# Kernel tuning notes

Hardware: AMD Instinct MI355X
Metric: run time of the kernel (lower is better)

The kernel has to match this reference:

```python
import jax, jax.numpy as jnp
import numpy as np
from jax import lax

BETA = 0.9
THRESHOLD = 1.0
SLOPE = 25.0
TIME_STEPS = 50


@jax.custom_vjp
def spike(u):
    # Heaviside forward; fast_sigmoid surrogate backward
    return (u > 0).astype(u.dtype)

def _spike_fwd(u):
    return spike(u), u

def _spike_bwd(u, g):
    return (g / (SLOPE * jnp.abs(u) + 1.0) ** 2,)

spike.defvjp(_spike_fwd, _spike_bwd)


def setup_inputs() -> dict:
    key = jax.random.key(0)
    k = jax.random.split(key, 5)
    B, D_IN, D_H, D_OUT = 1024, 1024, 2048, 256
    return {
        "x": jax.random.normal(k[0], (B, D_IN), jnp.float32),
        "W1": jax.random.normal(k[1], (D_H, D_IN), jnp.float32) / np.sqrt(D_IN),
        "b1": jax.random.normal(k[2], (D_H,), jnp.float32) * 0.01,
        "W2": jax.random.normal(k[3], (D_OUT, D_H), jnp.float32) / np.sqrt(D_H),
        "b2": jax.random.normal(k[4], (D_OUT,), jnp.float32) * 0.01,
    }


def reference(x, W1, b1, W2, b2):
    # fc1(x) is constant across time steps (static input) -> hoist out of scan
    cur1 = x @ W1.T + b1  # [B, H]
    B = x.shape[0]
    H, O = W1.shape[0], W2.shape[0]
    dt = x.dtype

    def step(carry, _):
        mem1, mem2, h_sum, out_sum = carry
        # snntorch Leaky, subtract reset: reset based on PREVIOUS mem, detached
        reset1 = lax.stop_gradient((mem1 > THRESHOLD).astype(dt))
        mem1 = BETA * mem1 + cur1 - reset1 * THRESHOLD
        spk1 = spike(mem1 - THRESHOLD)
        cur2 = spk1 @ W2.T + b2  # [B, O]
        reset2 = lax.stop_gradient((mem2 > THRESHOLD).astype(dt))
        mem2 = BETA * mem2 + cur2 - reset2 * THRESHOLD
        spk2 = spike(mem2 - THRESHOLD)
        return (mem1, mem2, h_sum + spk1, out_sum + spk2), None

    init = (jnp.zeros((B, H), dt), jnp.zeros((B, O), dt),
            jnp.zeros((B, H), dt), jnp.zeros((B, O), dt))
    (mem1, mem2, h_sum, out_sum), _ = lax.scan(step, init, None, length=TIME_STEPS)
    return (h_sum, out_sum)
```

## Files before the change

kernel.cpp:

```cpp
#include <hip/hip_runtime.h>
#include <stdint.h>


#define BATCH 1024
#define DIN   1024
#define DH    2048
#define DOUT  256
#define TSTEPS 50
#define QS    131072.0f
#define QINVS 7.62939453125e-6f

typedef __bf16 bf16x8 __attribute__((ext_vector_type(8)));
typedef float  f32x4  __attribute__((ext_vector_type(4)));
typedef int    i32x4  __attribute__((ext_vector_type(4)));
typedef int    i32x16 __attribute__((ext_vector_type(16)));

__device__ __forceinline__ uint16_t f32_bf16_rne(float f) {
  uint32_t u = __float_as_uint(f);
  uint32_t r = u + 0x7FFFu + ((u >> 16) & 1u);
  return (uint16_t)(r >> 16);
}

__device__ __forceinline__ i32x4 expand16(uint32_t s) {
  i32x4 r;
  r[0] = (int)((( s        & 0xFu) * 0x00204081u) & 0x01010101u);
  r[1] = (int)((((s >>  4) & 0xFu) * 0x00204081u) & 0x01010101u);
  r[2] = (int)((((s >>  8) & 0xFu) * 0x00204081u) & 0x01010101u);
  r[3] = (int)((((s >> 12) & 0xFu) * 0x00204081u) & 0x01010101u);
  return r;
}

__global__ void prep_kernel(const float* __restrict__ x, const float* __restrict__ W1,
                            const float* __restrict__ W2,
                            uint16_t* __restrict__ PXh, uint16_t* __restrict__ PXl,
                            uint16_t* __restrict__ PWh, uint16_t* __restrict__ PWl,
                            int8_t* __restrict__ PB) {
  int bid = blockIdx.x;
  if (bid < 1536) {
    const float* src;
    uint16_t *dh, *dl;
    int m, ko; size_t M;
    if (bid < 512) {
      int t = bid * 256 + threadIdx.x;
      m = t & 1023; ko = t >> 10; M = 1024;
      src = x + (size_t)m * DIN + ko * 8;
      dh = PXh; dl = PXl;
    } else {
      int t = (bid - 512) * 256 + threadIdx.x;
      m = t & 2047; ko = t >> 11; M = 2048;
      src = W1 + (size_t)m * DIN + ko * 8;
      dh = PWh; dl = PWl;
    }
    float4 a = *(const float4*)(src);
    float4 b = *(const float4*)(src + 4);
    float v[8] = {a.x, a.y, a.z, a.w, b.x, b.y, b.z, b.w};
    uint16_t h[8], l[8];
#pragma unroll
    for (int j = 0; j < 8; ++j) {
      h[j] = f32_bf16_rne(v[j]);
      l[j] = f32_bf16_rne(v[j] - __uint_as_float((uint32_t)h[j] << 16));
    }
    size_t o = ((size_t)ko * M + m) * 8;
    *(uint4*)(dh + o) = make_uint4(h[0] | (h[1] << 16), h[2] | (h[3] << 16),
                                   h[4] | (h[5] << 16), h[6] | (h[7] << 16));
    *(uint4*)(dl + o) = make_uint4(l[0] | (l[1] << 16), l[2] | (l[3] << 16),
                                   l[4] | (l[5] << 16), l[6] | (l[7] << 16));
  } else {
    int t = (bid - 1536) * 256 + threadIdx.x;
    int n = t & 255;
    int k0 = (t >> 8) * 16;
    uint32_t hw[4], lw[4];
#pragma unroll
    for (int g = 0; g < 4; ++g) {
      float4 v = *(const float4*)(W2 + (size_t)n * DH + k0 + g * 4);
      float vv[4] = {v.x, v.y, v.z, v.w};
      uint32_t hb = 0, lb = 0;
#pragma unroll
      for (int j = 0; j < 4; ++j) {
        int q = (int)rintf(vv[j] * QS);
        int h = (q + 128) >> 8;
        int l = q - (h << 8);
        hb |= ((uint32_t)(uint8_t)(int8_t)h) << (8 * j);
        lb |= ((uint32_t)(uint8_t)(int8_t)l) << (8 * j);
      }
      hw[g] = hb; lw[g] = lb;
    }
    int kc = k0 >> 5, kh = (k0 >> 4) & 1, nb = n >> 5;
    int lane = (n & 31) + 32 * kh;
    size_t off = (((size_t)(kc * 8 + nb) * 2 + 0) * 64 + lane) * 16;
    *(uint4*)(PB + off)        = make_uint4(hw[0], hw[1], hw[2], hw[3]);
    *(uint4*)(PB + off + 1024) = make_uint4(lw[0], lw[1], lw[2], lw[3]);
  }
}

__global__ __launch_bounds__(256, 2) void gemm1_kernel(
    const uint16_t* __restrict__ PXh, const uint16_t* __restrict__ PXl,
    const uint16_t* __restrict__ PWh, const uint16_t* __restrict__ PWl,
    const float* __restrict__ bias, float* __restrict__ C) {
  const int N = DH;
  int tid = threadIdx.x;
  int lane = tid & 63, wave = tid >> 6;
  int wm = (wave >> 1) * 32, wn = (wave & 1) * 32;
  int m0 = blockIdx.x * 64 + wm;
  int n0 = blockIdx.y * 64 + wn;
  int rf = lane & 15;
  int ko = lane >> 4;
  const int AK = 4 * 1024 * 8;
  const int BK = 4 * 2048 * 8;

  const uint16_t* axh = PXh + ((size_t)ko * 1024 + m0 + rf) * 8;
  const uint16_t* axl = PXl + ((size_t)ko * 1024 + m0 + rf) * 8;
  const uint16_t* bwh = PWh + ((size_t)ko * 2048 + n0 + rf) * 8;
  const uint16_t* bwl = PWl + ((size_t)ko * 2048 + n0 + rf) * 8;

  f32x4 acc[2][2] = {};
  bf16x8 ah[2][2], al[2][2], bh[2][2], bl[2][2];
#pragma unroll
  for (int s = 0; s < 2; ++s) {
#pragma unroll
    for (int i = 0; i < 2; ++i) {
      ah[s][i] = *(const bf16x8*)(axh + i * 128);
      al[s][i] = *(const bf16x8*)(axl + i * 128);
      bh[s][i] = *(const bf16x8*)(bwh + i * 128);
      bl[s][i] = *(const bf16x8*)(bwl + i * 128);
    }
    axh += AK; axl += AK; bwh += BK; bwl += BK;
  }
  __builtin_amdgcn_sched_barrier(0);

  for (int kc0 = 0; kc0 < 32; kc0 += 2) {
#pragma unroll
    for (int u = 0; u < 2; ++u) {
#pragma unroll
      for (int i = 0; i < 2; ++i)
#pragma unroll
        for (int j = 0; j < 2; ++j) {
          acc[i][j] = __builtin_amdgcn_mfma_f32_16x16x32_bf16(ah[u][i], bh[u][j], acc[i][j], 0, 0, 0);
          acc[i][j] = __builtin_amdgcn_mfma_f32_16x16x32_bf16(ah[u][i], bl[u][j], acc[i][j], 0, 0, 0);
          acc[i][j] = __builtin_amdgcn_mfma_f32_16x16x32_bf16(al[u][i], bh[u][j], acc[i][j], 0, 0, 0);
        }
      __builtin_amdgcn_sched_barrier(0);
#pragma unroll
      for (int i = 0; i < 2; ++i) {
        ah[u][i] = *(const bf16x8*)(axh + i * 128);
        al[u][i] = *(const bf16x8*)(axl + i * 128);
        bh[u][i] = *(const bf16x8*)(bwh + i * 128);
        bl[u][i] = *(const bf16x8*)(bwl + i * 128);
      }
      axh += AK; axl += AK; bwh += BK; bwl += BK;
      __builtin_amdgcn_sched_barrier(0);
    }
  }

  int cq = (lane >> 4) * 4;
#pragma unroll
  for (int j = 0; j < 2; ++j) {
    int col = n0 + j * 16 + rf;
    float bv = bias[col];
#pragma unroll
    for (int i = 0; i < 2; ++i) {
      size_t row = m0 + i * 16 + cq;
      float* cp = C + row * N + col;
#pragma unroll
      for (int r = 0; r < 4; ++r) cp[(size_t)r * N] = acc[i][j][r] + bv;
    }
  }
}

__global__ __launch_bounds__(256, 3) void gemm2_kernel(
    const uint16_t* __restrict__ PAb, const int8_t* __restrict__ PB,
    const float* __restrict__ bias, float* __restrict__ C, int RB) {
  int tid = threadIdx.x;
  int lane = tid & 63, wave = tid >> 6;
  int bxm = blockIdx.x;
  int nb  = blockIdx.y;

  const uint16_t* pa = PAb + (size_t)(bxm * 8 + wave * 2) * 64 + lane;
  const int8_t*   pb = PB + ((size_t)nb * 2 * 64 + lane) * 16;
  size_t strideA = (size_t)RB * 64;

  i32x16 acch[2] = {};
  i32x16 accl[2] = {};

  uint16_t abit[4][2];
  i32x4 bbh[4], bbl[4];
  i32x4 aexp[2][2];

#pragma unroll
  for (int u = 0; u < 4; ++u) {
#pragma unroll
    for (int mi = 0; mi < 2; ++mi) abit[u][mi] = pa[mi * 64];
    bbh[u] = *(const i32x4*)(pb);
    bbl[u] = *(const i32x4*)(pb + 1024);
    pa += strideA; pb += 16384;
  }
#pragma unroll
  for (int mi = 0; mi < 2; ++mi) aexp[0][mi] = expand16(abit[0][mi]);
  __builtin_amdgcn_sched_barrier(0);

  for (int kc0 = 0; kc0 < 64; kc0 += 4) {
#pragma unroll
    for (int u = 0; u < 4; ++u) {
      const int p = u & 1;
#pragma unroll
      for (int mi = 0; mi < 2; ++mi) aexp[p ^ 1][mi] = expand16(abit[(u + 1) & 3][mi]);
#pragma unroll
      for (int mi = 0; mi < 2; ++mi) {
        acch[mi] = __builtin_amdgcn_mfma_i32_32x32x32_i8(aexp[p][mi], bbh[u], acch[mi], 0, 0, 0);
        accl[mi] = __builtin_amdgcn_mfma_i32_32x32x32_i8(aexp[p][mi], bbl[u], accl[mi], 0, 0, 0);
      }
      __builtin_amdgcn_sched_barrier(0);
#pragma unroll
      for (int mi = 0; mi < 2; ++mi) abit[u][mi] = pa[mi * 64];
      bbh[u] = *(const i32x4*)(pb);
      bbl[u] = *(const i32x4*)(pb + 1024);
      pa += strideA; pb += 16384;
      __builtin_amdgcn_sched_barrier(0);
    }
  }

  int rm = lane & 31, half = lane >> 5;
  int col = nb * 32 + rm;
  float bv = bias[col];
#pragma unroll
  for (int mi = 0; mi < 2; ++mi) {
#pragma unroll
    for (int r = 0; r < 16; ++r) {
      int row = bxm * 256 + wave * 64 + mi * 32 + (r & 3) + 8 * (r >> 2) + 4 * half;
      int q = acch[mi][r] * 256 + accl[mi][r];
      C[(size_t)row * DOUT + col] = (float)q * QINVS + bv;
    }
  }
}

__global__ void lif1_kernel(const float* __restrict__ cur1, float* __restrict__ mem1,
                            uint16_t* __restrict__ PAb, float* __restrict__ hsum,
                            int tc, int init, int save_mem, int RB) {
#pragma clang fp contract(off)
  int idx = blockIdx.x * 256 + threadIdx.x;
  int b = idx & 1023;
  int h0 = (idx >> 10) * 16;
  size_t e0 = (size_t)b * DH + h0;

  float m[16], c[16], hs[16];
#pragma unroll
  for (int g = 0; g < 4; ++g) {
    float4 v = *(const float4*)(cur1 + e0 + g * 4);
    c[g * 4] = v.x; c[g * 4 + 1] = v.y; c[g * 4 + 2] = v.z; c[g * 4 + 3] = v.w;
  }
#pragma unroll
  for (int v = 0; v < 16; ++v) { m[v] = 0.0f; hs[v] = 0.0f; }
  if (!init) {
#pragma unroll
    for (int g = 0; g < 4; ++g) {
      float4 v = *(const float4*)(mem1 + e0 + g * 4);
      m[g * 4] = v.x; m[g * 4 + 1] = v.y; m[g * 4 + 2] = v.z; m[g * 4 + 3] = v.w;
    }
  }

  int kc = h0 >> 5, kh = (h0 >> 4) & 1;
  int lane = (b & 31) + 32 * kh;
  uint16_t* pab = PAb + ((size_t)kc * RB + (b >> 5)) * 64 + lane;

  for (int t = 0; t < tc; ++t) {
    uint32_t w = 0;
#pragma unroll
    for (int v = 0; v < 16; ++v) {
      float r = (m[v] > 1.0f) ? 1.0f : 0.0f;
      m[v] = 0.9f * m[v] + c[v] - r;
      bool s = (m[v] - 1.0f) > 0.0f;
      hs[v] += s ? 1.0f : 0.0f;
      w |= (s ? 1u : 0u) << v;
    }
    *pab = (uint16_t)w;
    pab += 32 * 64;
  }

  if (save_mem) {
#pragma unroll
    for (int g = 0; g < 4; ++g)
      *(float4*)(mem1 + e0 + g * 4) = make_float4(m[g * 4], m[g * 4 + 1], m[g * 4 + 2], m[g * 4 + 3]);
  }
  if (init) {
#pragma unroll
    for (int g = 0; g < 4; ++g)
      *(float4*)(hsum + e0 + g * 4) = make_float4(hs[g * 4], hs[g * 4 + 1], hs[g * 4 + 2], hs[g * 4 + 3]);
  } else {
#pragma unroll
    for (int g = 0; g < 4; ++g) {
      float4 v = *(float4*)(hsum + e0 + g * 4);
      v.x += hs[g * 4]; v.y += hs[g * 4 + 1]; v.z += hs[g * 4 + 2]; v.w += hs[g * 4 + 3];
      *(float4*)(hsum + e0 + g * 4) = v;
    }
  }
}

__global__ void lif2_kernel(const float* __restrict__ cur2, float* __restrict__ mem2,
                            float* __restrict__ osum, int tc, int init, int save_mem) {
#pragma clang fp contract(off)
  int idx = blockIdx.x * 256 + threadIdx.x;
  int e = idx * 4;
  float m[4], os[4];
  if (init) { m[0] = m[1] = m[2] = m[3] = 0.0f; }
  else { float4 v = *(const float4*)(mem2 + e); m[0] = v.x; m[1] = v.y; m[2] = v.z; m[3] = v.w; }
  os[0] = os[1] = os[2] = os[3] = 0.0f;
  for (int t = 0; t < tc; ++t) {
    float4 cv = *(const float4*)(cur2 + (size_t)t * (BATCH * DOUT) + e);
    float c[4] = {cv.x, cv.y, cv.z, cv.w};
#pragma unroll
    for (int v = 0; v < 4; ++v) {
      float r = (m[v] > 1.0f) ? 1.0f : 0.0f;
      m[v] = 0.9f * m[v] + c[v] - r;
      os[v] += ((m[v] - 1.0f) > 0.0f) ? 1.0f : 0.0f;
    }
  }
  if (save_mem) *(float4*)(mem2 + e) = make_float4(m[0], m[1], m[2], m[3]);
  if (init) {
    *(float4*)(osum + e) = make_float4(os[0], os[1], os[2], os[3]);
  } else {
    float4 v = *(float4*)(osum + e);
    v.x += os[0]; v.y += os[1]; v.z += os[2]; v.w += os[3];
    *(float4*)(osum + e) = v;
  }
}

extern "C" void kernel_launch(void* const* d_in, const int* in_sizes, int n_in,
                              void* d_out, int out_size, void* d_ws, size_t ws_size,
                              hipStream_t stream) {
  const float* x  = (const float*)d_in[0];
  const float* W1 = (const float*)d_in[1];
  const float* b1 = (const float*)d_in[2];
  const float* W2 = (const float*)d_in[3];
  const float* b2 = (const float*)d_in[4];
  float* out = (float*)d_out;
  char* ws = (char*)d_ws;

  const size_t fixed = 36 * 1024 * 1024;
  const size_t perT  = 262144 + 1048576;
  int tc = 10;
  if (ws_size >= fixed + 50ull * perT) tc = 50;
  else if (ws_size >= fixed + 25ull * perT) tc = 25;
  int nchunk = TSTEPS / tc;
  int RB = tc * 32;

  size_t off = 0;
  auto alloc = [&](size_t b) { size_t p = off; off = (off + b + 255) & ~(size_t)255; return p; };
  uint16_t* PXh  = (uint16_t*)(ws + alloc(2097152));
  uint16_t* PXl  = (uint16_t*)(ws + alloc(2097152));
  uint16_t* PWh  = (uint16_t*)(ws + alloc(4194304));
  uint16_t* PWl  = (uint16_t*)(ws + alloc(4194304));
  int8_t*   PB   = (int8_t*)(ws + alloc(1048576 + 262144));
  float*    cur1 = (float*)(ws + alloc(8388608));
  float*    mem1 = (float*)(ws + alloc(8388608));
  float*    mem2 = (float*)(ws + alloc(1048576));
  uint16_t* PAb  = (uint16_t*)(ws + alloc((size_t)tc * 262144 + 4ull * RB * 128));
  float*    cur2c = (float*)(ws + alloc((size_t)tc * BATCH * DOUT * 4));

  if (nchunk > 1) {
    hipMemsetAsync(mem1, 0, 8388608, stream);
    hipMemsetAsync(mem2, 0, 1048576, stream);
  }

  prep_kernel<<<1664, 256, 0, stream>>>(x, W1, W2, PXh, PXl, PWh, PWl, PB);

  gemm1_kernel<<<dim3(16, 32), 256, 0, stream>>>(PXh, PXl, PWh, PWl, b1, cur1);

  int save = (nchunk > 1) ? 1 : 0;
  for (int c = 0; c < nchunk; ++c) {
    int init = (c == 0) ? 1 : 0;
    lif1_kernel<<<(BATCH * DH) / (256 * 16), 256, 0, stream>>>(
        cur1, mem1, PAb, out, tc, init, save, RB);
    gemm2_kernel<<<dim3((tc * BATCH) / 256, 8), 256, 0, stream>>>(
        PAb, PB, b2, cur2c, RB);
    lif2_kernel<<<(BATCH * DOUT) / (256 * 4), 256, 0, stream>>>(
        cur2c, mem2, out + BATCH * DH, tc, init, save);
  }
}
```

Baseline: 195.6 us.

## Fuse layer-1 GEMM with LIF time loop via shared-memory epilogue

Adds a gemm1lif kernel that computes the fc1 tile, stages it with bias in shared memory, then runs the 50-step layer-1 LIF recurrence in registers, writing packed spike bits and hidden spike counts directly. This removes the round trip of the 8 MB cur1 tensor through global memory and one kernel launch when all time steps fit in a single chunk. The multi-chunk path keeps the old separate kernels. The GEMM blocks now carry a serial 50-step epilogue and extra shared memory, which may affect occupancy.

```diff
diff --git a/kernel.cpp b/kernel.cpp
--- a/kernel.cpp
+++ b/kernel.cpp
@@ -93,6 +93,119 @@
   }
 }
 
+__global__ __launch_bounds__(256, 2) void gemm1lif_kernel(
+    const uint16_t* __restrict__ PXh, const uint16_t* __restrict__ PXl,
+    const uint16_t* __restrict__ PWh, const uint16_t* __restrict__ PWl,
+    const float* __restrict__ bias, uint16_t* __restrict__ PAb,
+    float* __restrict__ hsum, int RB) {
+  __shared__ float sC[64 * 68];
+  int tid = threadIdx.x;
+  int lane = tid & 63, wave = tid >> 6;
+  int wm = (wave >> 1) * 32, wn = (wave & 1) * 32;
+  int m0blk = blockIdx.x * 64, n0blk = blockIdx.y * 64;
+  int m0 = m0blk + wm, n0 = n0blk + wn;
+  int rf = lane & 15;
+  int ko = lane >> 4;
+  const int AK = 4 * 1024 * 8;
+  const int BK = 4 * 2048 * 8;
+
+  const uint16_t* axh = PXh + ((size_t)ko * 1024 + m0 + rf) * 8;
+  const uint16_t* axl = PXl + ((size_t)ko * 1024 + m0 + rf) * 8;
+  const uint16_t* bwh = PWh + ((size_t)ko * 2048 + n0 + rf) * 8;
+  const uint16_t* bwl = PWl + ((size_t)ko * 2048 + n0 + rf) * 8;
+
+  f32x4 acc[2][2] = {};
+  bf16x8 ah[2][2], al[2][2], bh[2][2], bl[2][2];
+#pragma unroll
+  for (int s = 0; s < 2; ++s) {
+#pragma unroll
+    for (int i = 0; i < 2; ++i) {
+      ah[s][i] = *(const bf16x8*)(axh + i * 128);
+      al[s][i] = *(const bf16x8*)(axl + i * 128);
+      bh[s][i] = *(const bf16x8*)(bwh + i * 128);
+      bl[s][i] = *(const bf16x8*)(bwl + i * 128);
+    }
+    axh += AK; axl += AK; bwh += BK; bwl += BK;
+  }
+  __builtin_amdgcn_sched_barrier(0);
+
+  for (int kc0 = 0; kc0 < 32; kc0 += 2) {
+#pragma unroll
+    for (int u = 0; u < 2; ++u) {
+#pragma unroll
+      for (int i = 0; i < 2; ++i)
+#pragma unroll
+        for (int j = 0; j < 2; ++j) {
+          acc[i][j] = __builtin_amdgcn_mfma_f32_16x16x32_bf16(ah[u][i], bh[u][j], acc[i][j], 0, 0, 0);
+          acc[i][j] = __builtin_amdgcn_mfma_f32_16x16x32_bf16(ah[u][i], bl[u][j], acc[i][j], 0, 0, 0);
+          acc[i][j] = __builtin_amdgcn_mfma_f32_16x16x32_bf16(al[u][i], bh[u][j], acc[i][j], 0, 0, 0);
+        }
+      __builtin_amdgcn_sched_barrier(0);
+#pragma unroll
+      for (int i = 0; i < 2; ++i) {
+        ah[u][i] = *(const bf16x8*)(axh + i * 128);
+        al[u][i] = *(const bf16x8*)(axl + i * 128);
+        bh[u][i] = *(const bf16x8*)(bwh + i * 128);
+        bl[u][i] = *(const bf16x8*)(bwl + i * 128);
+      }
+      axh += AK; axl += AK; bwh += BK; bwl += BK;
+      __builtin_amdgcn_sched_barrier(0);
+    }
+  }
+
+  int cq = (lane >> 4) * 4;
+#pragma unroll
+  for (int j = 0; j < 2; ++j) {
+    int colL = wn + j * 16 + rf;
+    float bv = bias[n0blk + colL];
+#pragma unroll
+    for (int i = 0; i < 2; ++i) {
+      int rowL = wm + i * 16 + cq;
+#pragma unroll
+      for (int r = 0; r < 4; ++r)
+        sC[(rowL + r) * 68 + colL] = acc[i][j][r] + bv;
+    }
+  }
+  __syncthreads();
+
+  {
+#pragma clang fp contract(off)
+    int bL = tid & 63, hg = tid >> 6;
+    int b = m0blk + bL;
+    int h0 = n0blk + hg * 16;
+    float c[16], m[16], hs[16];
+#pragma unroll
+    for (int g = 0; g < 4; ++g) {
+      float4 v = *(const float4*)&sC[bL * 68 + hg * 16 + g * 4];
+      c[g * 4] = v.x; c[g * 4 + 1] = v.y; c[g * 4 + 2] = v.z; c[g * 4 + 3] = v.w;
+    }
+#pragma unroll
+    for (int v = 0; v < 16; ++v) { m[v] = 0.0f; hs[v] = 0.0f; }
+
+    int kc = h0 >> 5, kh = (h0 >> 4) & 1;
+    int laneP = (b & 31) + 32 * kh;
+    uint16_t* pab = PAb + ((size_t)kc * RB + (b >> 5)) * 64 + laneP;
+
+    for (int t = 0; t < TSTEPS; ++t) {
+      uint32_t w = 0;
+#pragma unroll
+      for (int v = 0; v < 16; ++v) {
+        float r = (m[v] > 1.0f) ? 1.0f : 0.0f;
+        m[v] = 0.9f * m[v] + c[v] - r;
+        bool s = (m[v] - 1.0f) > 0.0f;
+        hs[v] += s ? 1.0f : 0.0f;
+        w |= (s ? 1u : 0u) << v;
+      }
+      *pab = (uint16_t)w;
+      pab += 32 * 64;
+    }
+#pragma unroll
+    for (int g = 0; g < 4; ++g)
+      *(float4*)(hsum + (size_t)b * DH + h0 + g * 4) =
+          make_float4(hs[g * 4], hs[g * 4 + 1], hs[g * 4 + 2], hs[g * 4 + 3]);
+  }
+}
+
 __global__ __launch_bounds__(256, 2) void gemm1_kernel(
     const uint16_t* __restrict__ PXh, const uint16_t* __restrict__ PXl,
     const uint16_t* __restrict__ PWh, const uint16_t* __restrict__ PWl,
@@ -356,23 +469,24 @@
   uint16_t* PAb  = (uint16_t*)(ws + alloc((size_t)tc * 262144 + 4ull * RB * 128));
   float*    cur2c = (float*)(ws + alloc((size_t)tc * BATCH * DOUT * 4));
 
-  if (nchunk > 1) {
+  prep_kernel<<<1664, 256, 0, stream>>>(x, W1, W2, PXh, PXl, PWh, PWl, PB);
+
+  if (nchunk == 1) {
+    gemm1lif_kernel<<<dim3(16, 32), 256, 0, stream>>>(PXh, PXl, PWh, PWl, b1, PAb, out, RB);
+    gemm2_kernel<<<dim3((tc * BATCH) / 256, 8), 256, 0, stream>>>(PAb, PB, b2, cur2c, RB);
+    lif2_kernel<<<(BATCH * DOUT) / (256 * 4), 256, 0, stream>>>(
+        cur2c, mem2, out + BATCH * DH, tc, 1, 0);
+  } else {
     hipMemsetAsync(mem1, 0, 8388608, stream);
     hipMemsetAsync(mem2, 0, 1048576, stream);
-  }
-
-  prep_kernel<<<1664, 256, 0, stream>>>(x, W1, W2, PXh, PXl, PWh, PWl, PB);
-
-  gemm1_kernel<<<dim3(16, 32), 256, 0, stream>>>(PXh, PXl, PWh, PWl, b1, cur1);
-
-  int save = (nchunk > 1) ? 1 : 0;
-  for (int c = 0; c < nchunk; ++c) {
-    int init = (c == 0) ? 1 : 0;
-    lif1_kernel<<<(BATCH * DH) / (256 * 16), 256, 0, stream>>>(
-        cur1, mem1, PAb, out, tc, init, save, RB);
-    gemm2_kernel<<<dim3((tc * BATCH) / 256, 8), 256, 0, stream>>>(
-        PAb, PB, b2, cur2c, RB);
-    lif2_kernel<<<(BATCH * DOUT) / (256 * 4), 256, 0, stream>>>(
-        cur2c, mem2, out + BATCH * DH, tc, init, save);
-  }
-}
+    gemm1_kernel<<<dim3(16, 32), 256, 0, stream>>>(PXh, PXl, PWh, PWl, b1, cur1);
+    for (int c = 0; c < nchunk; ++c) {
+      int init = (c == 0) ? 1 : 0;
+      lif1_kernel<<<(BATCH * DH) / (256 * 16), 256, 0, stream>>>(
+          cur1, mem1, PAb, out, tc, init, 1, RB);
+      gemm2_kernel<<<dim3((tc * BATCH) / 256, 8), 256, 0, stream>>>(PAb, PB, b2, cur2c, RB);
+      lif2_kernel<<<(BATCH * DOUT) / (256 * 4), 256, 0, stream>>>(
+          cur2c, mem2, out + BATCH * DH, tc, init, 1);
+    }
+  }
+}
```

New measurement: 186.9 us (median of 2 runs). 4.4% less time.
